# Kernel optimization log

Hardware: AMD Instinct MI355X
Metric: run time of the kernel (lower is better)

The kernel has to match this reference:

```python
import jax, jax.numpy as jnp
import numpy as np

B, N, D, H, L, R = 2, 2048, 1024, 16, 3, 2
HID = int(D * 2.67)
NASH_ITERS, SINK_ITERS = 3, 10
EPS = 1e-6


def _rmsnorm(x, w):
    return x * w * jax.lax.rsqrt(jnp.mean(x * x, axis=-1, keepdims=True) + EPS)


def _sinkhorn(logits):
    # Sinkhorn-Knopp projection of exp(logits) to a doubly-stochastic matrix
    M = jnp.exp(logits)
    for _ in range(SINK_ITERS):
        M = M / jnp.sum(M, axis=1, keepdims=True)
        M = M / jnp.sum(M, axis=0, keepdims=True)
    return M


def _swiglu(x, wg, wu, wd):
    return (jax.nn.silu(x @ wg) * (x @ wu)) @ wd


def _attention(xl, wq, wk, Wv):
    # causal multi-head attention at one scale; V projection (Wv) is shared across scales
    b, n, d = xl.shape
    dh = d // H
    q = (xl @ wq).reshape(b, n, H, dh)
    k = (xl @ wk).reshape(b, n, H, dh)
    v = (xl @ Wv).reshape(b, n, H, dh)
    scores = jnp.einsum('bqhd,bkhd->bhqk', q, k) / jnp.asarray(float(np.sqrt(dh)), xl.dtype)
    mask = jnp.tril(jnp.ones((n, n), bool))
    scores = jnp.where(mask, scores, jnp.asarray(-1e9, xl.dtype))
    p = jax.nn.softmax(scores, axis=-1)
    return jnp.einsum('bhqk,bkhd->bqhd', p, v).reshape(b, n, d)


def _forward(x, norm_attn_w, norm_ffn_w, W_dec, Wq, Wk, Wv, Wo, agg_logits,
             w_gate, w_up, w_down, mhc_attn_logits, mhc_ffn_logits):
    residual = x
    xn = _rmsnorm(x, norm_attn_w)
    # 1) hierarchical decomposition: avg-pool by R each level, per-scale projection
    scales = []
    cur = xn
    for l in range(L):
        scales.append(cur @ W_dec[l])
        if l < L - 1:
            b, n, d = cur.shape
            cur = cur.reshape(b, n // R, R, d).mean(axis=2)
    # 2) multiscale causal attention with shared V; upsample back to N and project
    outs = []
    for l in range(L):
        o = _attention(scales[l], Wq[l], Wk[l], Wv)
        o = jnp.repeat(o, R ** l, axis=1)  # [B, N, D]
        outs.append(o @ Wo)
    Y = jnp.stack(outs, axis=0)  # [L, B, N, D]
    # 3) Nash aggregation: best-response iterations on scale weights
    w = jax.nn.softmax(agg_logits)
    for _ in range(NASH_ITERS):
        y_bar = jnp.einsum('l,lbnd->bnd', w, Y)
        u = -jnp.mean((Y - y_bar[None]) ** 2, axis=(1, 2, 3))  # [L] payoffs
        w = jax.nn.softmax(agg_logits + u)
    attn_out = jnp.einsum('l,lbnd->bnd', w, Y)
    aux_loss = jnp.sum(w * jnp.log(w * L + 1e-9))  # KL(w || uniform)
    # 4) mHC residual mixing (attention branch): doubly-stochastic convex mix
    P = _sinkhorn(mhc_attn_logits)
    x = P[0, 0] * residual + P[0, 1] * attn_out
    # 5) SwiGLU FFN + mHC residual (FFN branch)
    residual = x
    xn = _rmsnorm(x, norm_ffn_w)
    ffn_out = _swiglu(xn, w_gate, w_up, w_down)
    P2 = _sinkhorn(mhc_ffn_logits)
    x = P2[0, 0] * residual + P2[0, 1] * ffn_out
    return x, aux_loss


def setup_inputs() -> dict:
    key = jax.random.key(0)
    ks = jax.random.split(key, 16)
    init = 0.02
    s = lambda i, shape: jax.random.normal(ks[i], shape, jnp.float32) * init
    return {
        'x': jax.random.normal(ks[0], (B, N, D), jnp.float32),
        'norm_attn_w': jnp.ones((D,), jnp.float32),
        'norm_ffn_w': jnp.ones((D,), jnp.float32),
        'W_dec': s(1, (L, D, D)),
        'Wq': s(2, (L, D, D)),
        'Wk': s(3, (L, D, D)),
        'Wv': s(4, (D, D)),
        'Wo': s(5, (D, D)),
        'agg_logits': jnp.zeros((L,), jnp.float32),
        'w_gate': s(6, (D, HID)),
        'w_up': s(7, (D, HID)),
        'w_down': s(8, (HID, D)),
        'mhc_attn_logits': jnp.zeros((2, 2), jnp.float32),
        'mhc_ffn_logits': jnp.zeros((2, 2), jnp.float32),
    }


def reference(x, norm_attn_w, norm_ffn_w, W_dec, Wq, Wk, Wv, Wo, agg_logits,
              w_gate, w_up, w_down, mhc_attn_logits, mhc_ffn_logits):
    return _forward(x, norm_attn_w, norm_ffn_w, W_dec, Wq, Wk, Wv, Wo, agg_logits,
                    w_gate, w_up, w_down, mhc_attn_logits, mhc_ffn_logits)
```

## Files before the change

kernel.cpp:

```cpp
#include <hip/hip_runtime.h>
#include <stdint.h>


#define B_   2
#define N_   2048
#define D_   1024
#define H_   16
#define DH_  64
#define HID_ 2734
#define HIDP 2816
#define CNT  (B_*N_*D_)
#define LOG2E 1.4426950408889634f

typedef unsigned short u16;
typedef __attribute__((ext_vector_type(8))) short short8;
typedef __attribute__((ext_vector_type(4))) float f32x4;
typedef __attribute__((ext_vector_type(4))) uint16_t u16x4;

__device__ __forceinline__ u16 f2bf(float f) {
  uint32_t u = __builtin_bit_cast(uint32_t, f);
  u += 0x7fffu + ((u >> 16) & 1u);
  return (u16)(u >> 16);
}
__device__ __forceinline__ float bf2f(u16 h) {
  uint32_t u = ((uint32_t)h) << 16;
  return __builtin_bit_cast(float, u);
}
__device__ __forceinline__ uint32_t pkbf(float a, float b) {
  return (uint32_t)f2bf(a) | ((uint32_t)f2bf(b) << 16);
}
__device__ __forceinline__ void gload_lds16(const void* g, void* l) {
  __builtin_amdgcn_global_load_lds(
      (const __attribute__((address_space(1))) uint32_t*)g,
      (__attribute__((address_space(3))) uint32_t*)l, 16, 0, 0);
}

__global__ __launch_bounds__(256) void wprep_k(const float* __restrict__ Wdec, const float* __restrict__ Wq,
                                               const float* __restrict__ Wk, const float* __restrict__ Wv,
                                               const float* __restrict__ Wo, const float* __restrict__ Wg,
                                               const float* __restrict__ Wu, const float* __restrict__ Wdn,
                                               u16* __restrict__ A_wp, u16* __restrict__ WdecB,
                                               u16* __restrict__ WoT, u16* __restrict__ BTgu,
                                               u16* __restrict__ WdnT, float* __restrict__ SCb) {
  const int bid = blockIdx.x;
  if (bid >= 21760) {
    int bid0 = bid - 21760;
    int row = (bid0 < 2) ? (5454 + bid0) : (5470 + (bid0 - 2));
    u16x4 zz; zz[0]=0; zz[1]=0; zz[2]=0; zz[3]=0;
    *(u16x4*)(BTgu + (size_t)row*1024 + threadIdx.x*4) = zz;
    return;
  }
  if (bid >= 18688) {
    if (bid == 18688 && threadIdx.x < 64) SCb[threadIdx.x] = 0.f;
    int i = (bid - 18688)*1024 + threadIdx.x*4;
    float4 v = *(const float4*)(Wdec + i);
    u16x4 o; o[0]=f2bf(v.x); o[1]=f2bf(v.y); o[2]=f2bf(v.z); o[3]=f2bf(v.w);
    *(u16x4*)(WdecB + i) = o;
    return;
  }
  const float* src; u16* dst; int K, N, KP; float scale; int imode; int bx, by;
  if (bid < 9216) {
    int j = bid >> 10, t = bid & 1023; bx = t & 31; by = t >> 5;
    int l = j / 3, which = j - l*3;
    src = which==0 ? Wq + (size_t)l*1048576 : which==1 ? Wk + (size_t)l*1048576 : Wv;
    dst = A_wp + (size_t)(l*3072 + which*1024)*1024;
    K = 1024; N = 1024; KP = 1024; scale = (which==0) ? 0.125f*LOG2E : 1.f; imode = 0;
  } else if (bid < 10240) {
    int t = bid - 9216; bx = t & 31; by = t >> 5;
    src = Wo; dst = WoT; K=1024; N=1024; KP=1024; scale=1.f; imode=0;
  } else if (bid < 13056) {
    int t = bid - 10240; bx = t % 88; by = t / 88;
    src = Wg; dst = BTgu; K=1024; N=HID_; KP=1024; scale=1.f; imode=1;
  } else if (bid < 15872) {
    int t = bid - 13056; bx = t % 88; by = t / 88;
    src = Wu; dst = BTgu; K=1024; N=HID_; KP=1024; scale=1.f; imode=2;
  } else {
    int t = bid - 15872; bx = t & 31; by = t >> 5;
    src = Wdn; dst = WdnT; K=HID_; N=1024; KP=HIDP; scale=1.f; imode=0;
  }
  __shared__ float tt[32][33];
  const int tx = threadIdx.x & 31, ty = threadIdx.x >> 5;
  const int nb = bx*32, kb = by*32;
  #pragma unroll
  for (int i = 0; i < 4; i++) {
    int k = kb + ty + i*8, n = nb + tx;
    tt[ty + i*8][tx] = (k < K && n < N) ? src[(size_t)k * N + n] * scale : 0.f;
  }
  __syncthreads();
  #pragma unroll
  for (int i = 0; i < 4; i++) {
    int n = nb + ty + i*8, k = kb + tx;
    int r;
    if (imode == 0) r = n;
    else if (imode == 1) r = ((n>>4)<<5) + (n&15);
    else r = ((n>>4)<<5) + 16 + (n&15);
    dst[(size_t)r * KP + k] = f2bf(tt[tx][ty + i*8]);
  }
}

__global__ __launch_bounds__(256) void rmsA_k(const float* __restrict__ x, const float* __restrict__ w,
                                              u16* __restrict__ xn, u16* __restrict__ xp1) {
  const int j = blockIdx.x;
  const float* xr0 = x + (size_t)(2*j) * D_;
  const float* xr1 = xr0 + D_;
  float a0[4], a1[4], wv[4];
  float ss0 = 0.f, ss1 = 0.f;
  #pragma unroll
  for (int i = 0; i < 4; i++) {
    int c = threadIdx.x + i*256;
    a0[i] = xr0[c]; a1[i] = xr1[c]; wv[i] = w[c];
    ss0 += a0[i]*a0[i]; ss1 += a1[i]*a1[i];
  }
  #pragma unroll
  for (int o = 1; o < 64; o <<= 1) { ss0 += __shfl_xor(ss0, o); ss1 += __shfl_xor(ss1, o); }
  __shared__ float r0[4], r1[4];
  if ((threadIdx.x & 63) == 0) { r0[threadIdx.x >> 6] = ss0; r1[threadIdx.x >> 6] = ss1; }
  __syncthreads();
  float sc0 = rsqrtf((r0[0]+r0[1]+r0[2]+r0[3]) * (1.f/D_) + 1e-6f);
  float sc1 = rsqrtf((r1[0]+r1[1]+r1[2]+r1[3]) * (1.f/D_) + 1e-6f);
  #pragma unroll
  for (int i = 0; i < 4; i++) {
    int c = threadIdx.x + i*256;
    float xa = a0[i]*wv[i]*sc0, xb = a1[i]*wv[i]*sc1;
    xn[(size_t)(2*j)*D_ + c]     = f2bf(xa);
    xn[(size_t)(2*j)*D_ + D_ + c] = f2bf(xb);
    xp1[(size_t)j*D_ + c] = f2bf(0.5f*(xa + xb));
  }
}

__global__ __launch_bounds__(256) void pool_k(const u16* __restrict__ in, u16* __restrict__ out, int lg) {
  const int No = 1 << lg;
  const int total4 = B_ * No * 256;
  for (int i = blockIdx.x*256 + threadIdx.x; i < total4; i += gridDim.x*256) {
    int d4 = i & 255; int j = (i >> 8) & (No - 1); int b = i >> (8 + lg);
    size_t src = ((size_t)(b*2*No + 2*j) << 10) + d4*4;
    u16x4 a = *(const u16x4*)(in + src);
    u16x4 c = *(const u16x4*)(in + src + 1024);
    u16x4 o;
    #pragma unroll
    for (int t = 0; t < 4; t++) o[t] = f2bf(0.5f * (bf2f(a[t]) + bf2f(c[t])));
    *(u16x4*)(out + (size_t)i*4) = o;
  }
}

template<int MT, int MODE>
__global__ __launch_bounds__(256, 2) void gemm_t(const u16* __restrict__ A, const u16* __restrict__ BT,
                                                 void* __restrict__ Cv, void* __restrict__ Cv2,
                                                 const float* __restrict__ X1,
                                                 const float* __restrict__ SCp,
                                                 int N, int K, int t1, int t2, unsigned int bt_stride) {
  static_assert(MT == 4, "counted vmcnt(8) assumes MT+4 == 8 staging loads");
  __shared__ __align__(16) u16 As[2][MT*32*64];
  __shared__ __align__(16) u16 Bs[2][128*64];
  const int tid = threadIdx.x;
  const int lane = tid & 63, wid = tid >> 6;
  const int quad = lane >> 4, c16 = lane & 15;
  const int y = blockIdx.y;
  const int m0 = y * (MT*32), n0 = blockIdx.x * 128;
  const int wm = wid >> 1, wn = wid & 1;
  const int level = (y >= t2) ? 2 : ((y >= t1) ? 1 : 0);
  BT += (size_t)level * bt_stride;

  f32x4 acc[MT][4];
  #pragma unroll
  for (int i = 0; i < MT; i++)
    #pragma unroll
    for (int j = 0; j < 4; j++) acc[i][j] = f32x4{0.f,0.f,0.f,0.f};

  const int srow = lane >> 3;
  const int schunk = lane & 7;
  auto stage = [&](int k0, int p) {
    #pragma unroll
    for (int t = 0; t < MT; t++) {
      int idx = wid*MT + t;
      int row = idx*8 + srow;
      int g = (schunk ^ (row & 7)) * 8;
      gload_lds16(A + (size_t)(m0+row)*K + k0 + g, &As[p][idx*512]);
    }
    #pragma unroll
    for (int t = 0; t < 4; t++) {
      int idx = wid*4 + t;
      int row = idx*8 + srow;
      int g = (schunk ^ (row & 7)) * 8;
      gload_lds16(BT + (size_t)(n0+row)*K + k0 + g, &Bs[p][idx*512]);
    }
  };

  const int nk = K >> 6;
  stage(0, 0);
  for (int ki = 0; ki < nk; ki++) {
    const int p = ki & 1;
    if (ki + 1 < nk) {
      stage((ki + 1) << 6, p ^ 1);
      asm volatile("s_waitcnt vmcnt(8)" ::: "memory");
    } else {
      asm volatile("s_waitcnt vmcnt(0)" ::: "memory");
    }
    __builtin_amdgcn_s_barrier();
    __builtin_amdgcn_sched_barrier(0);
    __builtin_amdgcn_s_setprio(1);
    #pragma unroll
    for (int kh = 0; kh < 2; kh++) {
      short8 af[MT], bfr[4];
      #pragma unroll
      for (int mt = 0; mt < MT; mt++) {
        int ar = wm*(MT*16) + mt*16 + c16;
        int ck = (kh*4 + quad) ^ (ar & 7);
        af[mt] = *(const short8*)(&As[p][ar*64 + ck*8]);
      }
      #pragma unroll
      for (int nt = 0; nt < 4; nt++) {
        int br = wn*64 + nt*16 + c16;
        int ck = (kh*4 + quad) ^ (br & 7);
        bfr[nt] = *(const short8*)(&Bs[p][br*64 + ck*8]);
      }
      #pragma unroll
      for (int mt = 0; mt < MT; mt++)
        #pragma unroll
        for (int nt = 0; nt < 4; nt++)
          acc[mt][nt] = __builtin_amdgcn_mfma_f32_16x16x32_bf16(af[mt], bfr[nt], acc[mt][nt], 0, 0, 0);
    }
    __builtin_amdgcn_s_setprio(0);
    __builtin_amdgcn_sched_barrier(0);
    __builtin_amdgcn_s_barrier();
  }
  if (MODE == 1) {
    u16* C = (u16*)Cv;
    #pragma unroll
    for (int mt = 0; mt < MT; mt++)
      #pragma unroll
      for (int nt = 0; nt < 4; nt++)
        #pragma unroll
        for (int r = 0; r < 4; r++) {
          int row = m0 + wm*(MT*16) + mt*16 + quad*4 + r;
          int col = n0 + wn*64 + nt*16 + c16;
          C[(size_t)row * N + col] = f2bf(acc[mt][nt][r]);
        }
  } else if (MODE == 2) {
    float* C = (float*)Cv;
    const float q0 = SCp[11], q1 = SCp[12];
    #pragma unroll
    for (int mt = 0; mt < MT; mt++)
      #pragma unroll
      for (int nt = 0; nt < 4; nt++)
        #pragma unroll
        for (int r = 0; r < 4; r++) {
          int row = m0 + wm*(MT*16) + mt*16 + quad*4 + r;
          int col = n0 + wn*64 + nt*16 + c16;
          size_t o = (size_t)row * N + col;
          C[o] = q0 * X1[o] + q1 * acc[mt][nt][r];
        }
  } else if (MODE == 3) {
    u16* Hc = (u16*)Cv;
    const int hbase = (n0 >> 1) + wn*32;
    #pragma unroll
    for (int mt = 0; mt < MT; mt++)
      #pragma unroll
      for (int r = 0; r < 4; r++) {
        int row = m0 + wm*(MT*16) + mt*16 + quad*4 + r;
        #pragma unroll
        for (int pr = 0; pr < 2; pr++) {
          float g = acc[mt][2*pr][r], u = acc[mt][2*pr+1][r];
          float h = g / (1.f + __expf(-g)) * u;
          Hc[(size_t)row * HIDP + hbase + pr*16 + c16] = f2bf(h);
        }
      }
  } else {
    if (n0 < 2048) {
      u16* C = (u16*)Cv;
      #pragma unroll
      for (int mt = 0; mt < MT; mt++)
        #pragma unroll
        for (int nt = 0; nt < 4; nt++)
          #pragma unroll
          for (int r = 0; r < 4; r++) {
            int row = m0 + wm*(MT*16) + mt*16 + quad*4 + r;
            int col = n0 + wn*64 + nt*16 + c16;
            C[(size_t)row * N + col] = f2bf(acc[mt][nt][r]);
          }
    } else {
      const int Nl = 2048 >> level;
      const int lvbase = (level==0) ? 0 : (level==1) ? 4096 : 6144;
      const size_t vtoff = (level==0) ? 0 : (level==1) ? 4194304 : 6291456;
      u16* VT = (u16*)Cv2 + vtoff;
      #pragma unroll
      for (int mt = 0; mt < MT; mt++) {
        int rowg = m0 + wm*(MT*16) + mt*16 + quad*4;
        int nloc = rowg - lvbase;
        int b = nloc / Nl;
        int n = nloc - b*Nl;
        #pragma unroll
        for (int nt = 0; nt < 4; nt++) {
          int c = n0 - 2048 + wn*64 + nt*16 + c16;
          u16x4 o;
          o[0]=f2bf(acc[mt][nt][0]); o[1]=f2bf(acc[mt][nt][1]);
          o[2]=f2bf(acc[mt][nt][2]); o[3]=f2bf(acc[mt][nt][3]);
          *(u16x4*)(VT + ((size_t)(b*1024 + c))*Nl + n) = o;
        }
      }
    }
  }
}

__global__ __launch_bounds__(256) void flash_k(const u16* __restrict__ QKVg,
                                               const u16* __restrict__ VTg,
                                               u16* __restrict__ Og) {
  __shared__ __align__(16) u16 Kt[2][64*64];
  __shared__ __align__(16) u16 Vt[2][64*64];
  __shared__ __align__(16) u16 Ps[4][32*68];
  const int tid = threadIdx.x, lane = tid & 63, wid = tid >> 6;
  const int quad = lane >> 4, c16 = lane & 15;
  const int id = blockIdx.x;
  int qt, bh, Nl, rowbase; size_t vtoff;
  if (id < 512)      { qt = 15 - (id >> 5);            bh = id & 31;  Nl = 2048; rowbase = 0;    vtoff = 0; }
  else if (id < 768) { int t2 = id - 512; qt = 7 - (t2 >> 5); bh = t2 & 31; Nl = 1024; rowbase = 4096; vtoff = 4194304; }
  else               { int t2 = id - 768; qt = 3 - (t2 >> 5); bh = t2 & 31; Nl = 512;  rowbase = 6144; vtoff = 6291456; }
  const int b = bh >> 4, h = bh & 15;
  const u16* QK = QKVg + ((size_t)(rowbase + b*Nl)) * 3072 + h*64;
  u16* Ow = Og + ((size_t)(rowbase + b*Nl)) * 1024 + h*64;
  const u16* VT = VTg + vtoff + ((size_t)b*1024 + h*64) * (size_t)Nl;

  const int q0r = qt*128 + wid*32;
  short8 bq[2][2];
  #pragma unroll
  for (int qh = 0; qh < 2; qh++) {
    const u16* qp = QK + (size_t)(q0r + qh*16 + c16)*3072 + quad*8;
    bq[qh][0] = *(const short8*)qp;
    bq[qh][1] = *(const short8*)(qp + 32);
  }
  const int si0 = wid*2, si1 = si0 + 1;
  const int sr0 = si0*8 + (lane>>3), sr1 = si1*8 + (lane>>3);
  const int sg  = ((lane&7) ^ (lane>>3)) * 8;
  const u16* Ks0 = QK + 1024 + (size_t)sr0*3072 + sg;
  const u16* Ks1 = QK + 1024 + (size_t)sr1*3072 + sg;
  const u16* Vs0 = VT + (size_t)sr0*Nl + sg;
  const u16* Vs1 = VT + (size_t)sr1*Nl + sg;

  f32x4 oacc[2][4];
  f32x4 lacc[2];
  #pragma unroll
  for (int qh = 0; qh < 2; qh++) {
    lacc[qh] = f32x4{0.f,0.f,0.f,0.f};
    #pragma unroll
    for (int nt = 0; nt < 4; nt++) oacc[qh][nt] = f32x4{0.f,0.f,0.f,0.f};
  }

  auto stage = [&](int kt, int p) {
    const size_t ko = (size_t)kt * 64;
    gload_lds16(Ks0 + ko*3072, &Kt[p][si0*512]);
    gload_lds16(Ks1 + ko*3072, &Kt[p][si1*512]);
    gload_lds16(Vs0 + ko,      &Vt[p][si0*512]);
    gload_lds16(Vs1 + ko,      &Vt[p][si1*512]);
  };
  const int kmax_w = 2*qt + (wid >> 1);
  const int ktot   = 2*qt + 2;
  stage(0, 0);

  for (int kt = 0; kt < ktot; kt++) {
    const int p = kt & 1;
    __syncthreads();
    if (kt + 1 < ktot) stage(kt+1, p^1);
    if (kt > kmax_w) continue;

    f32x4 st[2][4];
    #pragma unroll
    for (int nt = 0; nt < 4; nt++) {
      int key = nt*16 + c16, x = key & 7;
      short8 a0 = *(const short8*)(&Kt[p][key*64 + ((quad    ) ^ x)*8]);
      short8 a1 = *(const short8*)(&Kt[p][key*64 + ((quad + 4) ^ x)*8]);
      #pragma unroll
      for (int qh = 0; qh < 2; qh++) {
        f32x4 s = f32x4{0.f,0.f,0.f,0.f};
        s = __builtin_amdgcn_mfma_f32_16x16x32_bf16(a0, bq[qh][0], s, 0, 0, 0);
        s = __builtin_amdgcn_mfma_f32_16x16x32_bf16(a1, bq[qh][1], s, 0, 0, 0);
        st[qh][nt] = s;
      }
    }
    if (kt >= 2*qt) {
      const int kb = kt*64;
      #pragma unroll
      for (int qh = 0; qh < 2; qh++) {
        const int qr = q0r + qh*16 + c16;
        #pragma unroll
        for (int nt = 0; nt < 4; nt++) {
          #pragma unroll
          for (int r = 0; r < 4; r++) {
            float e = __builtin_amdgcn_exp2f(st[qh][nt][r]);
            st[qh][nt][r] = (kb + nt*16 + quad*4 + r <= qr) ? e : 0.f;
          }
          lacc[qh] += st[qh][nt];
        }
      }
    } else {
      #pragma unroll
      for (int qh = 0; qh < 2; qh++)
        #pragma unroll
        for (int nt = 0; nt < 4; nt++) {
          #pragma unroll
          for (int r = 0; r < 4; r++) st[qh][nt][r] = __builtin_amdgcn_exp2f(st[qh][nt][r]);
          lacc[qh] += st[qh][nt];
        }
    }
    #pragma unroll
    for (int qh = 0; qh < 2; qh++) {
      const int prow = qh*16 + c16;
      #pragma unroll
      for (int nt = 0; nt < 4; nt++) {
        uint2 pk;
        pk.x = pkbf(st[qh][nt][0], st[qh][nt][1]);
        pk.y = pkbf(st[qh][nt][2], st[qh][nt][3]);
        *(uint2*)(&Ps[wid][prow*68 + nt*16 + quad*4]) = pk;
      }
    }
    short8 bp[2][2];
    #pragma unroll
    for (int qh = 0; qh < 2; qh++) {
      bp[qh][0] = *(const short8*)(&Ps[wid][(qh*16 + c16)*68 +      quad*8]);
      bp[qh][1] = *(const short8*)(&Ps[wid][(qh*16 + c16)*68 + 32 + quad*8]);
    }
    #pragma unroll
    for (int nt = 0; nt < 4; nt++) {
      int dh = nt*16 + c16, x = dh & 7;
      short8 a0 = *(const short8*)(&Vt[p][dh*64 + ((quad    ) ^ x)*8]);
      short8 a1 = *(const short8*)(&Vt[p][dh*64 + ((quad + 4) ^ x)*8]);
      #pragma unroll
      for (int qh = 0; qh < 2; qh++) {
        oacc[qh][nt] = __builtin_amdgcn_mfma_f32_16x16x32_bf16(a0, bp[qh][0], oacc[qh][nt], 0, 0, 0);
        oacc[qh][nt] = __builtin_amdgcn_mfma_f32_16x16x32_bf16(a1, bp[qh][1], oacc[qh][nt], 0, 0, 0);
      }
    }
  }
  #pragma unroll
  for (int qh = 0; qh < 2; qh++) {
    float ls = lacc[qh][0] + lacc[qh][1] + lacc[qh][2] + lacc[qh][3];
    ls += __shfl_xor(ls, 16);
    ls += __shfl_xor(ls, 32);
    const float rl = 1.f / ls;
    #pragma unroll
    for (int nt = 0; nt < 4; nt++) {
      uint2 o;
      o.x = pkbf(oacc[qh][nt][0]*rl, oacc[qh][nt][1]*rl);
      o.y = pkbf(oacc[qh][nt][2]*rl, oacc[qh][nt][3]*rl);
      *(uint2*)(Ow + (size_t)(q0r + qh*16 + c16)*1024 + nt*16 + quad*4) = o;
    }
  }
}

__global__ __launch_bounds__(256) void gram_k(const u16* __restrict__ Y0, const u16* __restrict__ Y1,
                                              const u16* __restrict__ Y2, float* __restrict__ G) {
  float a[6] = {0,0,0,0,0,0};
  const int total4 = CNT/4;
  for (int i = blockIdx.x*256 + threadIdx.x; i < total4; i += gridDim.x*256) {
    int d4 = i & 255; int n = (i >> 8) & (N_-1); int b = i >> 19;
    u16x4 y0v = *(const u16x4*)(Y0 + (size_t)i*4);
    u16x4 y1v = *(const u16x4*)(Y1 + (((size_t)(b*1024 + (n>>1))) << 10) + d4*4);
    u16x4 y2v = *(const u16x4*)(Y2 + (((size_t)(b*512  + (n>>2))) << 10) + d4*4);
    #pragma unroll
    for (int t = 0; t < 4; t++) {
      float y0 = bf2f(y0v[t]), y1 = bf2f(y1v[t]), y2 = bf2f(y2v[t]);
      a[0] += y0*y0; a[1] += y0*y1; a[2] += y0*y2;
      a[3] += y1*y1; a[4] += y1*y2; a[5] += y2*y2;
    }
  }
  __shared__ float red[4][6];
  const int lane = threadIdx.x & 63, wid = threadIdx.x >> 6;
  #pragma unroll
  for (int t = 0; t < 6; t++) {
    float v = a[t];
    v += __shfl_xor(v, 1);  v += __shfl_xor(v, 2);  v += __shfl_xor(v, 4);
    v += __shfl_xor(v, 8);  v += __shfl_xor(v, 16); v += __shfl_xor(v, 32);
    a[t] = v;
  }
  if (lane == 0)
    #pragma unroll
    for (int t = 0; t < 6; t++) red[wid][t] = a[t];
  __syncthreads();
  if (threadIdx.x < 6)
    atomicAdd(&G[threadIdx.x], red[0][threadIdx.x] + red[1][threadIdx.x] +
                               red[2][threadIdx.x] + red[3][threadIdx.x]);
}

__global__ void head_k(float* SC, const float* __restrict__ agg, const float* __restrict__ mA,
                       const float* __restrict__ mF, float* __restrict__ aux_out) {
  if (threadIdx.x != 0 || blockIdx.x != 0) return;
  float G[6];
  for (int t = 0; t < 6; t++) G[t] = SC[t];
  const int gi[3][3] = {{0,1,2},{1,3,4},{2,4,5}};
  float a[3] = {agg[0], agg[1], agg[2]};
  float w[3];
  {
    float m = fmaxf(a[0], fmaxf(a[1], a[2])); float s = 0.f;
    for (int l = 0; l < 3; l++) { w[l] = expf(a[l]-m); s += w[l]; }
    for (int l = 0; l < 3; l++) w[l] /= s;
  }
  const float inv = 1.f / (float)CNT;
  for (int it = 0; it < 3; it++) {
    float q = 0.f;
    for (int l = 0; l < 3; l++) for (int m2 = 0; m2 < 3; m2++) q += w[l]*w[m2]*G[gi[l][m2]];
    float z[3];
    for (int l = 0; l < 3; l++) {
      float dot = w[0]*G[gi[l][0]] + w[1]*G[gi[l][1]] + w[2]*G[gi[l][2]];
      z[l] = a[l] - (G[gi[l][l]] - 2.f*dot + q) * inv;
    }
    float m = fmaxf(z[0], fmaxf(z[1], z[2])); float s = 0.f;
    for (int l = 0; l < 3; l++) { w[l] = expf(z[l]-m); s += w[l]; }
    for (int l = 0; l < 3; l++) w[l] /= s;
  }
  SC[6] = w[0]; SC[7] = w[1]; SC[8] = w[2];
  aux_out[0] = w[0]*logf(w[0]*3.f + 1e-9f) + w[1]*logf(w[1]*3.f + 1e-9f) + w[2]*logf(w[2]*3.f + 1e-9f);
  for (int which = 0; which < 2; which++) {
    const float* Lg = which ? mF : mA;
    float M0 = expf(Lg[0]), M1 = expf(Lg[1]), M2 = expf(Lg[2]), M3 = expf(Lg[3]);
    for (int i2 = 0; i2 < 10; i2++) {
      float r0 = M0+M1, r1 = M2+M3; M0 /= r0; M1 /= r0; M2 /= r1; M3 /= r1;
      float c0 = M0+M2, c1 = M1+M3; M0 /= c0; M2 /= c0; M1 /= c1; M3 /= c1;
    }
    SC[9 + which*2] = M0; SC[10 + which*2] = M1;
  }
}

__global__ __launch_bounds__(256) void mixrms_k(const float* __restrict__ x, const u16* __restrict__ Y0,
                                                const u16* __restrict__ Y1, const u16* __restrict__ Y2,
                                                const float* __restrict__ SC, const float* __restrict__ w2,
                                                float* __restrict__ x1, u16* __restrict__ xn2) {
  const float w0 = SC[6], w1 = SC[7], ww2 = SC[8], p0 = SC[9], p1 = SC[10];
  const int i = blockIdx.x;
  const int b = i >> 11, n = i & 2047;
  const float* xr = x + (size_t)i * D_;
  const u16* y0 = Y0 + (size_t)i * D_;
  const u16* y1 = Y1 + (size_t)(b*1024 + (n>>1)) * D_;
  const u16* y2 = Y2 + (size_t)(b*512  + (n>>2)) * D_;
  float xv[4], wv[4];
  float ss = 0.f;
  #pragma unroll
  for (int t = 0; t < 4; t++) {
    int c = threadIdx.x + t*256;
    float v = p0*xr[c] + p1*(w0*bf2f(y0[c]) + w1*bf2f(y1[c]) + ww2*bf2f(y2[c]));
    xv[t] = v; wv[t] = w2[c]; ss += v*v;
    x1[(size_t)i*D_ + c] = v;
  }
  #pragma unroll
  for (int o = 1; o < 64; o <<= 1) ss += __shfl_xor(ss, o);
  __shared__ float red[4];
  if ((threadIdx.x & 63) == 0) red[threadIdx.x >> 6] = ss;
  __syncthreads();
  float sc = rsqrtf((red[0]+red[1]+red[2]+red[3]) * (1.f/D_) + 1e-6f);
  #pragma unroll
  for (int t = 0; t < 4; t++) {
    int c = threadIdx.x + t*256;
    xn2[(size_t)i*D_ + c] = f2bf(xv[t]*wv[t]*sc);
  }
}

extern "C" void kernel_launch(void* const* d_in, const int* in_sizes, int n_in,
                              void* d_out, int out_size, void* d_ws, size_t ws_size,
                              hipStream_t stream) {
  (void)in_sizes; (void)n_in; (void)out_size; (void)ws_size;
  const float* x    = (const float*)d_in[0];
  const float* nw1  = (const float*)d_in[1];
  const float* nw2  = (const float*)d_in[2];
  const float* Wdec = (const float*)d_in[3];
  const float* Wq   = (const float*)d_in[4];
  const float* Wk   = (const float*)d_in[5];
  const float* Wv   = (const float*)d_in[6];
  const float* Wo   = (const float*)d_in[7];
  const float* agg  = (const float*)d_in[8];
  const float* Wg   = (const float*)d_in[9];
  const float* Wu   = (const float*)d_in[10];
  const float* Wdn  = (const float*)d_in[11];
  const float* mA   = (const float*)d_in[12];
  const float* mF   = (const float*)d_in[13];
  float* out = (float*)d_out;

  char* ws = (char*)d_ws;
  size_t off = 0;
  auto take = [&](size_t b) { size_t r = off; off += (b + 255) & ~(size_t)255; return r; };

  u16* A_wp  = (u16*)(ws + take((size_t)9216*1024*2));
  u16* WdecB = (u16*)(ws + take((size_t)3*1024*1024*2));
  u16* Wqkv  = (u16*)(ws + take((size_t)9216*1024*2));
  u16* BTgu  = (u16*)(ws + take((size_t)5632*1024*2));
  u16* WdnT  = (u16*)(ws + take((size_t)HIDP*1024*2));
  u16* WoT   = (u16*)(ws + take((size_t)1024*1024*2));
  u16* xn_all = (u16*)(ws + take((size_t)7168*1024*2));
  float* x1  = (float*)(ws + take((size_t)CNT*4));
  float* SCb = (float*)(ws + take(256));
  char*  big = ws + take(88080384);
  u16*   QKV   = (u16*)big;
  u16*   VTa   = (u16*)(big + 44040192);
  u16*   Ob    = (u16*)(big + 58720256);
  u16*   YC    = (u16*)(big + 73400320);
  u16*   hbuf  = (u16*)big;

  dim3 blk(256);
  const int BIG = 1 << 30;

  wprep_k<<<21924, blk, 0, stream>>>(Wdec, Wq, Wk, Wv, Wo, Wg, Wu, Wdn,
                                     A_wp, WdecB, WoT, BTgu, WdnT, SCb);
  gemm_t<4,1><<<dim3(8, 72), blk, 0, stream>>>(A_wp, WdecB, Wqkv, nullptr, nullptr, nullptr,
                                               1024, 1024, 24, 48, 1024u*1024u);
  rmsA_k<<<2048, blk, 0, stream>>>(x, nw1, xn_all, xn_all + (size_t)4096*1024);
  pool_k<<<512, blk, 0, stream>>>(xn_all + (size_t)4096*1024, xn_all + (size_t)6144*1024, 9);
  gemm_t<4,4><<<dim3(24, 56), blk, 0, stream>>>(xn_all, Wqkv, QKV, VTa, nullptr, nullptr,
                                                3072, 1024, 32, 48, 3072u*1024u);
  flash_k<<<896, blk, 0, stream>>>(QKV, VTa, Ob);
  gemm_t<4,1><<<dim3(8, 56), blk, 0, stream>>>(Ob, WoT, YC, nullptr, nullptr, nullptr,
                                               1024, 1024, BIG, BIG, 0u);
  u16* YC1 = YC + (size_t)4096*1024;
  u16* YC2 = YC + (size_t)6144*1024;
  gram_k<<<1024, blk, 0, stream>>>(YC, YC1, YC2, SCb);
  head_k<<<1, 64, 0, stream>>>(SCb, agg, mA, mF, out + CNT);
  mixrms_k<<<4096, blk, 0, stream>>>(x, YC, YC1, YC2, SCb, nw2, x1, xn_all);
  gemm_t<4,3><<<dim3(44, 32), blk, 0, stream>>>(xn_all, BTgu, hbuf, nullptr, nullptr, nullptr,
                                                5632, 1024, BIG, BIG, 0u);
  gemm_t<4,2><<<dim3(8, 32), blk, 0, stream>>>(hbuf, WdnT, out, nullptr, x1, SCb,
                                               1024, HIDP, BIG, BIG, 0u);
}
```

Measured before the change: 494.1 us.

## Fuse rmsnorm and pooling into weight prep, merge gram with head, shrink down-proj tile

The first RMSNorm and both pooling levels now run as extra blocks of the weight-prep kernel, each block handling four rows so it can emit all pooled outputs directly. The one-thread head kernel is folded into the gram reduction: the last block to finish, found through an atomic counter, computes it. The down-projection GEMM switches to a 64-row M tile with the matching vmcnt count, doubling its grid to 512 blocks. These changes remove three launches and add parallelism to the final GEMM, at the cost of a counter that depends on SCb having been zeroed first and a smaller tile with less data reuse.

```diff
diff --git a/kernel.cpp b/kernel.cpp
--- a/kernel.cpp
+++ b/kernel.cpp
@@ -41,18 +41,63 @@
                                                const float* __restrict__ Wu, const float* __restrict__ Wdn,
                                                u16* __restrict__ A_wp, u16* __restrict__ WdecB,
                                                u16* __restrict__ WoT, u16* __restrict__ BTgu,
-                                               u16* __restrict__ WdnT, float* __restrict__ SCb) {
+                                               u16* __restrict__ WdnT, float* __restrict__ SCb,
+                                               const float* __restrict__ x, const float* __restrict__ nw1,
+                                               u16* __restrict__ xn, u16* __restrict__ xp1,
+                                               u16* __restrict__ xp2) {
   const int bid = blockIdx.x;
+  const int tid = threadIdx.x;
+  if (bid >= 21924) {
+    const int j = bid - 21924;
+    const float* xr = x + (size_t)(4*j) * D_;
+    float a0[4], a1[4], a2[4], a3[4], wv[4];
+    float s0=0.f, s1=0.f, s2=0.f, s3=0.f;
+    #pragma unroll
+    for (int i = 0; i < 4; i++) {
+      int c = tid + i*256;
+      wv[i] = nw1[c];
+      a0[i] = xr[c]; a1[i] = xr[D_+c]; a2[i] = xr[2*D_+c]; a3[i] = xr[3*D_+c];
+      s0 += a0[i]*a0[i]; s1 += a1[i]*a1[i]; s2 += a2[i]*a2[i]; s3 += a3[i]*a3[i];
+    }
+    #pragma unroll
+    for (int o = 1; o < 64; o <<= 1) {
+      s0 += __shfl_xor(s0, o); s1 += __shfl_xor(s1, o);
+      s2 += __shfl_xor(s2, o); s3 += __shfl_xor(s3, o);
+    }
+    __shared__ float rr[4][4];
+    if ((tid & 63) == 0) { int w = tid >> 6; rr[w][0]=s0; rr[w][1]=s1; rr[w][2]=s2; rr[w][3]=s3; }
+    __syncthreads();
+    float m0v = rr[0][0]+rr[1][0]+rr[2][0]+rr[3][0];
+    float m1v = rr[0][1]+rr[1][1]+rr[2][1]+rr[3][1];
+    float m2v = rr[0][2]+rr[1][2]+rr[2][2]+rr[3][2];
+    float m3v = rr[0][3]+rr[1][3]+rr[2][3]+rr[3][3];
+    float c0 = rsqrtf(m0v*(1.f/D_) + 1e-6f), c1 = rsqrtf(m1v*(1.f/D_) + 1e-6f);
+    float c2 = rsqrtf(m2v*(1.f/D_) + 1e-6f), c3 = rsqrtf(m3v*(1.f/D_) + 1e-6f);
+    #pragma unroll
+    for (int i = 0; i < 4; i++) {
+      int c = tid + i*256;
+      float v0 = a0[i]*wv[i]*c0, v1 = a1[i]*wv[i]*c1;
+      float v2 = a2[i]*wv[i]*c2, v3 = a3[i]*wv[i]*c3;
+      xn[(size_t)(4*j)*D_ + c]        = f2bf(v0);
+      xn[(size_t)(4*j)*D_ + D_ + c]   = f2bf(v1);
+      xn[(size_t)(4*j)*D_ + 2*D_ + c] = f2bf(v2);
+      xn[(size_t)(4*j)*D_ + 3*D_ + c] = f2bf(v3);
+      xp1[(size_t)(2*j)*D_ + c]       = f2bf(0.5f*(v0 + v1));
+      xp1[(size_t)(2*j)*D_ + D_ + c]  = f2bf(0.5f*(v2 + v3));
+      xp2[(size_t)j*D_ + c]           = f2bf(0.25f*(v0 + v1 + v2 + v3));
+    }
+    return;
+  }
   if (bid >= 21760) {
     int bid0 = bid - 21760;
     int row = (bid0 < 2) ? (5454 + bid0) : (5470 + (bid0 - 2));
     u16x4 zz; zz[0]=0; zz[1]=0; zz[2]=0; zz[3]=0;
-    *(u16x4*)(BTgu + (size_t)row*1024 + threadIdx.x*4) = zz;
+    *(u16x4*)(BTgu + (size_t)row*1024 + tid*4) = zz;
     return;
   }
   if (bid >= 18688) {
-    if (bid == 18688 && threadIdx.x < 64) SCb[threadIdx.x] = 0.f;
-    int i = (bid - 18688)*1024 + threadIdx.x*4;
+    if (bid == 18688 && tid < 64) SCb[tid] = 0.f;
+    int i = (bid - 18688)*1024 + tid*4;
     float4 v = *(const float4*)(Wdec + i);
     u16x4 o; o[0]=f2bf(v.x); o[1]=f2bf(v.y); o[2]=f2bf(v.z); o[3]=f2bf(v.w);
     *(u16x4*)(WdecB + i) = o;
@@ -79,7 +124,7 @@
     src = Wdn; dst = WdnT; K=HID_; N=1024; KP=HIDP; scale=1.f; imode=0;
   }
   __shared__ float tt[32][33];
-  const int tx = threadIdx.x & 31, ty = threadIdx.x >> 5;
+  const int tx = tid & 31, ty = tid >> 5;
   const int nb = bx*32, kb = by*32;
   #pragma unroll
   for (int i = 0; i < 4; i++) {
@@ -98,58 +143,13 @@
   }
 }
 
-__global__ __launch_bounds__(256) void rmsA_k(const float* __restrict__ x, const float* __restrict__ w,
-                                              u16* __restrict__ xn, u16* __restrict__ xp1) {
-  const int j = blockIdx.x;
-  const float* xr0 = x + (size_t)(2*j) * D_;
-  const float* xr1 = xr0 + D_;
-  float a0[4], a1[4], wv[4];
-  float ss0 = 0.f, ss1 = 0.f;
-  #pragma unroll
-  for (int i = 0; i < 4; i++) {
-    int c = threadIdx.x + i*256;
-    a0[i] = xr0[c]; a1[i] = xr1[c]; wv[i] = w[c];
-    ss0 += a0[i]*a0[i]; ss1 += a1[i]*a1[i];
-  }
-  #pragma unroll
-  for (int o = 1; o < 64; o <<= 1) { ss0 += __shfl_xor(ss0, o); ss1 += __shfl_xor(ss1, o); }
-  __shared__ float r0[4], r1[4];
-  if ((threadIdx.x & 63) == 0) { r0[threadIdx.x >> 6] = ss0; r1[threadIdx.x >> 6] = ss1; }
-  __syncthreads();
-  float sc0 = rsqrtf((r0[0]+r0[1]+r0[2]+r0[3]) * (1.f/D_) + 1e-6f);
-  float sc1 = rsqrtf((r1[0]+r1[1]+r1[2]+r1[3]) * (1.f/D_) + 1e-6f);
-  #pragma unroll
-  for (int i = 0; i < 4; i++) {
-    int c = threadIdx.x + i*256;
-    float xa = a0[i]*wv[i]*sc0, xb = a1[i]*wv[i]*sc1;
-    xn[(size_t)(2*j)*D_ + c]     = f2bf(xa);
-    xn[(size_t)(2*j)*D_ + D_ + c] = f2bf(xb);
-    xp1[(size_t)j*D_ + c] = f2bf(0.5f*(xa + xb));
-  }
-}
-
-__global__ __launch_bounds__(256) void pool_k(const u16* __restrict__ in, u16* __restrict__ out, int lg) {
-  const int No = 1 << lg;
-  const int total4 = B_ * No * 256;
-  for (int i = blockIdx.x*256 + threadIdx.x; i < total4; i += gridDim.x*256) {
-    int d4 = i & 255; int j = (i >> 8) & (No - 1); int b = i >> (8 + lg);
-    size_t src = ((size_t)(b*2*No + 2*j) << 10) + d4*4;
-    u16x4 a = *(const u16x4*)(in + src);
-    u16x4 c = *(const u16x4*)(in + src + 1024);
-    u16x4 o;
-    #pragma unroll
-    for (int t = 0; t < 4; t++) o[t] = f2bf(0.5f * (bf2f(a[t]) + bf2f(c[t])));
-    *(u16x4*)(out + (size_t)i*4) = o;
-  }
-}
-
 template<int MT, int MODE>
 __global__ __launch_bounds__(256, 2) void gemm_t(const u16* __restrict__ A, const u16* __restrict__ BT,
                                                  void* __restrict__ Cv, void* __restrict__ Cv2,
                                                  const float* __restrict__ X1,
                                                  const float* __restrict__ SCp,
                                                  int N, int K, int t1, int t2, unsigned int bt_stride) {
-  static_assert(MT == 4, "counted vmcnt(8) assumes MT+4 == 8 staging loads");
+  static_assert(MT == 4 || MT == 2, "vmcnt count assumes MT+4 staging loads");
   __shared__ __align__(16) u16 As[2][MT*32*64];
   __shared__ __align__(16) u16 Bs[2][128*64];
   const int tid = threadIdx.x;
@@ -192,7 +192,8 @@
     const int p = ki & 1;
     if (ki + 1 < nk) {
       stage((ki + 1) << 6, p ^ 1);
-      asm volatile("s_waitcnt vmcnt(8)" ::: "memory");
+      if constexpr (MT == 4) asm volatile("s_waitcnt vmcnt(8)" ::: "memory");
+      else                   asm volatile("s_waitcnt vmcnt(6)" ::: "memory");
     } else {
       asm volatile("s_waitcnt vmcnt(0)" ::: "memory");
     }
@@ -446,8 +447,11 @@
   }
 }
 
-__global__ __launch_bounds__(256) void gram_k(const u16* __restrict__ Y0, const u16* __restrict__ Y1,
-                                              const u16* __restrict__ Y2, float* __restrict__ G) {
+__global__ __launch_bounds__(256) void gramhead_k(const u16* __restrict__ Y0, const u16* __restrict__ Y1,
+                                                  const u16* __restrict__ Y2, float* __restrict__ G,
+                                                  int* __restrict__ done,
+                                                  const float* __restrict__ agg, const float* __restrict__ mA,
+                                                  const float* __restrict__ mF, float* __restrict__ aux_out) {
   float a[6] = {0,0,0,0,0,0};
   const int total4 = CNT/4;
   for (int i = blockIdx.x*256 + threadIdx.x; i < total4; i += gridDim.x*256) {
@@ -478,44 +482,47 @@
   if (threadIdx.x < 6)
     atomicAdd(&G[threadIdx.x], red[0][threadIdx.x] + red[1][threadIdx.x] +
                                red[2][threadIdx.x] + red[3][threadIdx.x]);
-}
-
-__global__ void head_k(float* SC, const float* __restrict__ agg, const float* __restrict__ mA,
-                       const float* __restrict__ mF, float* __restrict__ aux_out) {
-  if (threadIdx.x != 0 || blockIdx.x != 0) return;
-  float G[6];
-  for (int t = 0; t < 6; t++) G[t] = SC[t];
-  const int gi[3][3] = {{0,1,2},{1,3,4},{2,4,5}};
-  float a[3] = {agg[0], agg[1], agg[2]};
-  float w[3];
-  {
-    float m = fmaxf(a[0], fmaxf(a[1], a[2])); float s = 0.f;
-    for (int l = 0; l < 3; l++) { w[l] = expf(a[l]-m); s += w[l]; }
-    for (int l = 0; l < 3; l++) w[l] /= s;
-  }
-  const float inv = 1.f / (float)CNT;
-  for (int it = 0; it < 3; it++) {
-    float q = 0.f;
-    for (int l = 0; l < 3; l++) for (int m2 = 0; m2 < 3; m2++) q += w[l]*w[m2]*G[gi[l][m2]];
-    float z[3];
-    for (int l = 0; l < 3; l++) {
-      float dot = w[0]*G[gi[l][0]] + w[1]*G[gi[l][1]] + w[2]*G[gi[l][2]];
-      z[l] = a[l] - (G[gi[l][l]] - 2.f*dot + q) * inv;
-    }
-    float m = fmaxf(z[0], fmaxf(z[1], z[2])); float s = 0.f;
-    for (int l = 0; l < 3; l++) { w[l] = expf(z[l]-m); s += w[l]; }
-    for (int l = 0; l < 3; l++) w[l] /= s;
-  }
-  SC[6] = w[0]; SC[7] = w[1]; SC[8] = w[2];
-  aux_out[0] = w[0]*logf(w[0]*3.f + 1e-9f) + w[1]*logf(w[1]*3.f + 1e-9f) + w[2]*logf(w[2]*3.f + 1e-9f);
-  for (int which = 0; which < 2; which++) {
-    const float* Lg = which ? mF : mA;
-    float M0 = expf(Lg[0]), M1 = expf(Lg[1]), M2 = expf(Lg[2]), M3 = expf(Lg[3]);
-    for (int i2 = 0; i2 < 10; i2++) {
-      float r0 = M0+M1, r1 = M2+M3; M0 /= r0; M1 /= r0; M2 /= r1; M3 /= r1;
-      float c0 = M0+M2, c1 = M1+M3; M0 /= c0; M2 /= c0; M1 /= c1; M3 /= c1;
-    }
-    SC[9 + which*2] = M0; SC[10 + which*2] = M1;
+  __threadfence();
+  __shared__ int lastf;
+  if (threadIdx.x == 0) lastf = (atomicAdd(done, 1) == (int)gridDim.x - 1);
+  __syncthreads();
+  if (lastf && threadIdx.x == 0) {
+    float Gv[6];
+    for (int t = 0; t < 6; t++)
+      Gv[t] = __hip_atomic_load(&G[t], __ATOMIC_RELAXED, __HIP_MEMORY_SCOPE_AGENT);
+    float* SC = G;
+    const int gi[3][3] = {{0,1,2},{1,3,4},{2,4,5}};
+    float av[3] = {agg[0], agg[1], agg[2]};
+    float w[3];
+    {
+      float m = fmaxf(av[0], fmaxf(av[1], av[2])); float s = 0.f;
+      for (int l = 0; l < 3; l++) { w[l] = expf(av[l]-m); s += w[l]; }
+      for (int l = 0; l < 3; l++) w[l] /= s;
+    }
+    const float inv = 1.f / (float)CNT;
+    for (int it = 0; it < 3; it++) {
+      float q = 0.f;
+      for (int l = 0; l < 3; l++) for (int m2 = 0; m2 < 3; m2++) q += w[l]*w[m2]*Gv[gi[l][m2]];
+      float z[3];
+      for (int l = 0; l < 3; l++) {
+        float dot = w[0]*Gv[gi[l][0]] + w[1]*Gv[gi[l][1]] + w[2]*Gv[gi[l][2]];
+        z[l] = av[l] - (Gv[gi[l][l]] - 2.f*dot + q) * inv;
+      }
+      float m = fmaxf(z[0], fmaxf(z[1], z[2])); float s = 0.f;
+      for (int l = 0; l < 3; l++) { w[l] = expf(z[l]-m); s += w[l]; }
+      for (int l = 0; l < 3; l++) w[l] /= s;
+    }
+    SC[6] = w[0]; SC[7] = w[1]; SC[8] = w[2];
+    aux_out[0] = w[0]*logf(w[0]*3.f + 1e-9f) + w[1]*logf(w[1]*3.f + 1e-9f) + w[2]*logf(w[2]*3.f + 1e-9f);
+    for (int which = 0; which < 2; which++) {
+      const float* Lg = which ? mF : mA;
+      float M0 = expf(Lg[0]), M1 = expf(Lg[1]), M2 = expf(Lg[2]), M3 = expf(Lg[3]);
+      for (int i2 = 0; i2 < 10; i2++) {
+        float r0 = M0+M1, r1 = M2+M3; M0 /= r0; M1 /= r0; M2 /= r1; M3 /= r1;
+        float c0 = M0+M2, c1 = M1+M3; M0 /= c0; M2 /= c0; M1 /= c1; M3 /= c1;
+      }
+      SC[9 + which*2] = M0; SC[10 + which*2] = M1;
+    }
   }
 }
 
@@ -592,15 +599,18 @@
   u16*   YC    = (u16*)(big + 73400320);
   u16*   hbuf  = (u16*)big;
 
+  u16* xp1 = xn_all + (size_t)4096*1024;
+  u16* xp2 = xn_all + (size_t)6144*1024;
+  int* done = (int*)SCb + 15;
+
   dim3 blk(256);
   const int BIG = 1 << 30;
 
-  wprep_k<<<21924, blk, 0, stream>>>(Wdec, Wq, Wk, Wv, Wo, Wg, Wu, Wdn,
-                                     A_wp, WdecB, WoT, BTgu, WdnT, SCb);
+  wprep_k<<<22948, blk, 0, stream>>>(Wdec, Wq, Wk, Wv, Wo, Wg, Wu, Wdn,
+                                     A_wp, WdecB, WoT, BTgu, WdnT, SCb,
+                                     x, nw1, xn_all, xp1, xp2);
   gemm_t<4,1><<<dim3(8, 72), blk, 0, stream>>>(A_wp, WdecB, Wqkv, nullptr, nullptr, nullptr,
                                                1024, 1024, 24, 48, 1024u*1024u);
-  rmsA_k<<<2048, blk, 0, stream>>>(x, nw1, xn_all, xn_all + (size_t)4096*1024);
-  pool_k<<<512, blk, 0, stream>>>(xn_all + (size_t)4096*1024, xn_all + (size_t)6144*1024, 9);
   gemm_t<4,4><<<dim3(24, 56), blk, 0, stream>>>(xn_all, Wqkv, QKV, VTa, nullptr, nullptr,
                                                 3072, 1024, 32, 48, 3072u*1024u);
   flash_k<<<896, blk, 0, stream>>>(QKV, VTa, Ob);
@@ -608,11 +618,10 @@
                                                1024, 1024, BIG, BIG, 0u);
   u16* YC1 = YC + (size_t)4096*1024;
   u16* YC2 = YC + (size_t)6144*1024;
-  gram_k<<<1024, blk, 0, stream>>>(YC, YC1, YC2, SCb);
-  head_k<<<1, 64, 0, stream>>>(SCb, agg, mA, mF, out + CNT);
+  gramhead_k<<<1024, blk, 0, stream>>>(YC, YC1, YC2, SCb, done, agg, mA, mF, out + CNT);
   mixrms_k<<<4096, blk, 0, stream>>>(x, YC, YC1, YC2, SCb, nw2, x1, xn_all);
   gemm_t<4,3><<<dim3(44, 32), blk, 0, stream>>>(xn_all, BTgu, hbuf, nullptr, nullptr, nullptr,
                                                 5632, 1024, BIG, BIG, 0u);
-  gemm_t<4,2><<<dim3(8, 32), blk, 0, stream>>>(hbuf, WdnT, out, nullptr, x1, SCb,
+  gemm_t<2,2><<<dim3(8, 64), blk, 0, stream>>>(hbuf, WdnT, out, nullptr, x1, SCb,
                                                1024, HIDP, BIG, BIG, 0u);
 }
```

Result: slower. 519.8 us (+5.2%).
